# Optimization experiments

Hardware: AMD Instinct MI355X
Metric: run time of the kernel (lower is better)

Reference implementation:

```python
import jax, jax.numpy as jnp
import numpy as np

B, S, E, H = 4, 2048, 2048, 16
D = E // H  # head_dim = 128


def setup_inputs() -> dict:
    key = jax.random.key(0)
    ks = jax.random.split(key, 10)
    sc = 1.0 / np.sqrt(E)
    x = jax.random.normal(ks[0], (B, S, E), dtype=jnp.float32)
    causal_mask = jnp.tril(jnp.ones((S, S), dtype=jnp.int32))  # 1 = keep, 0 = mask
    wq = jax.random.normal(ks[1], (E, E), dtype=jnp.float32) * sc
    bq = jax.random.normal(ks[2], (E,), dtype=jnp.float32) * sc
    wk = jax.random.normal(ks[3], (E, E), dtype=jnp.float32) * sc
    bk = jax.random.normal(ks[4], (E,), dtype=jnp.float32) * sc
    wv = jax.random.normal(ks[5], (E, E), dtype=jnp.float32) * sc
    bv = jax.random.normal(ks[6], (E,), dtype=jnp.float32) * sc
    wo = jax.random.normal(ks[7], (E, E), dtype=jnp.float32) * sc
    bo = jax.random.normal(ks[8], (E,), dtype=jnp.float32) * sc
    return {"x": x, "causal_mask": causal_mask, "wq": wq, "bq": bq,
            "wk": wk, "bk": bk, "wv": wv, "bv": bv, "wo": wo, "bo": bo}


def _split_heads(t):
    # [B,S,E] -> [B,H,S,D]
    return t.reshape(B, S, H, D).transpose(0, 2, 1, 3)


def reference(x, causal_mask, wq, bq, wk, bk, wv, bv, wo, bo):
    # torch Linear: y = x @ W.T + b
    q = _split_heads(x @ wq.T + bq)
    k = _split_heads(x @ wk.T + bk)
    v = _split_heads(x @ wv.T + bv)
    scale = 1.0 / jnp.sqrt(jnp.asarray(D, dtype=x.dtype))
    dots = jnp.einsum("bhqd,bhkd->bhqk", q, k) * scale
    dots = jnp.where(causal_mask == 0, jnp.asarray(-jnp.inf, dots.dtype), dots)
    attn = jax.nn.softmax(dots, axis=-1)
    ctx = jnp.einsum("bhqk,bhkd->bhqd", attn, v)
    ctx = ctx.transpose(0, 2, 1, 3).reshape(B, S, E)  # merge heads
    return ctx @ wo.T + bo
```

## Files before the change

### kernel.cpp

```cpp
#include <hip/hip_runtime.h>
#include <hip/hip_bf16.h>

#define B_ 4
#define S_ 2048
#define E_ 2048
#define H_ 16
#define D_ 128
#define M_ (B_*S_)

typedef __attribute__((ext_vector_type(8))) short short8;
typedef __attribute__((ext_vector_type(4))) float f32x4;

__device__ __forceinline__ unsigned short f2bf(float f) {
  union { __hip_bfloat16 h; unsigned short u; } c;
  c.h = __float2bfloat16(f);
  return c.u;
}

__device__ __forceinline__ void gld_lds16(const void* g, void* l) {
  __builtin_amdgcn_global_load_lds((const __attribute__((address_space(1))) void*)g,
                                   (__attribute__((address_space(3))) void*)l, 16, 0, 0);
}

__global__ __launch_bounds__(256) void cast_bf16_kernel(const float* __restrict__ in,
                                                        unsigned short* __restrict__ out,
                                                        int n4) {
  int i = blockIdx.x * 256 + threadIdx.x;
  if (i >= n4) return;
  float4 v = ((const float4*)in)[i];
  ushort4 o;
  o.x = f2bf(v.x); o.y = f2bf(v.y); o.z = f2bf(v.z); o.w = f2bf(v.w);
  ((ushort4*)out)[i] = o;
}

template <typename OutT, bool TR = false>
__global__ __launch_bounds__(256) void gemm_bt(const unsigned short* __restrict__ A,
                                               const unsigned short* __restrict__ W,
                                               const float* __restrict__ bias,
                                               OutT* __restrict__ C,
                                               int M, int N, int K, float oscale) {
  __shared__ unsigned short As[128 * 64];
  __shared__ unsigned short Bs[128 * 64];
  const int tid  = threadIdx.x;
  const int lane = tid & 63;
  const int wid  = tid >> 6;
  const int nwg = gridDim.x * gridDim.y;
  const int lin = blockIdx.x + gridDim.x * blockIdx.y;
  const int nl  = (lin & 7) * (nwg >> 3) + (lin >> 3);
  const int m0 = (nl / gridDim.x) * 128;
  const int n0 = (nl % gridDim.x) * 128;
  const int wr = (wid >> 1) * 64;
  const int wc = (wid & 1) * 64;
  const int lr  = lane & 15;
  const int lg  = lane >> 4;

  f32x4 acc[4][4];
#pragma unroll
  for (int i = 0; i < 4; i++)
#pragma unroll
    for (int j = 0; j < 4; j++) acc[i][j] = (f32x4){0.f, 0.f, 0.f, 0.f};

  const int rS = tid >> 3;
  const int uS = (tid & 7) ^ (rS & 7);
  const unsigned short* asrc = A + (size_t)(m0 + rS) * K + uS * 8;
  const unsigned short* bsrc = W + (size_t)(n0 + rS) * K + uS * 8;
  char* adst = (char*)As + wid * 1024;
  char* bdst = (char*)Bs + wid * 1024;

  const int swR = (lr & 7) << 4;

  for (int kt = 0; kt < K; kt += 64) {
#pragma unroll
    for (int p = 0; p < 4; ++p) {
      gld_lds16(asrc + kt + (size_t)(32 * p) * K, adst + p * 4096);
      gld_lds16(bsrc + kt + (size_t)(32 * p) * K, bdst + p * 4096);
    }
    __syncthreads();

#pragma unroll
    for (int kk = 0; kk < 2; kk++) {
      const int cb = ((kk * 4 + lg) << 4) ^ swR;
      short8 af[4], bf[4];
#pragma unroll
      for (int i = 0; i < 4; i++)
        af[i] = *(const short8*)((const char*)As + (wr + i * 16 + lr) * 128 + cb);
#pragma unroll
      for (int j = 0; j < 4; j++)
        bf[j] = *(const short8*)((const char*)Bs + (wc + j * 16 + lr) * 128 + cb);
#pragma unroll
      for (int i = 0; i < 4; i++)
#pragma unroll
        for (int j = 0; j < 4; j++) {
          if constexpr (TR)
            acc[i][j] = __builtin_amdgcn_mfma_f32_16x16x32_bf16(bf[j], af[i], acc[i][j], 0, 0, 0);
          else
            acc[i][j] = __builtin_amdgcn_mfma_f32_16x16x32_bf16(af[i], bf[j], acc[i][j], 0, 0, 0);
        }
    }
    __syncthreads();
  }

  if constexpr (TR) {
    const int lg4 = (lane >> 4) * 4;
#pragma unroll
    for (int j = 0; j < 4; j++) {
      const int gn = n0 + wc + j * 16 + lg4;
      const float4 bv4 = *(const float4*)&bias[gn];
#pragma unroll
      for (int i = 0; i < 4; i++) {
        const int gm = m0 + wr + i * 16 + lr;
#pragma unroll
        for (int r = 0; r < 4; r++) {
          const float v = (acc[i][j][r] + ((const float*)&bv4)[r]) * oscale;
          ((unsigned short*)C)[(size_t)(gn + r) * M + gm] = f2bf(v);
        }
      }
    }
  } else {
#pragma unroll
    for (int i = 0; i < 4; i++) {
      const int gm = m0 + wr + i * 16 + (lane >> 4) * 4;
#pragma unroll
      for (int j = 0; j < 4; j++) {
        const int gn = n0 + wc + j * 16 + lr;
        const float bv = bias[gn];
#pragma unroll
        for (int r = 0; r < 4; r++) {
          const float v = (acc[i][j][r] + bv) * oscale;
          if constexpr (sizeof(OutT) == 2)
            ((unsigned short*)C)[(size_t)(gm + r) * N + gn] = f2bf(v);
          else
            ((float*)C)[(size_t)(gm + r) * N + gn] = v;
        }
      }
    }
  }
}

__global__ __launch_bounds__(256, 4) void flash_attn(const unsigned short* __restrict__ Q,
                                                     const unsigned short* __restrict__ K,
                                                     const unsigned short* __restrict__ VT,
                                                     unsigned short* __restrict__ Ctx) {
  __shared__ unsigned short Ks[64 * 128];
  __shared__ unsigned short Vt[128 * 64];
  __shared__ unsigned short Pl[4 * 1024];

  const int tid  = threadIdx.x;
  const int lane = tid & 63;
  const int wid  = tid >> 6;
  const int lr  = lane & 15;
  const int lg  = lane >> 4;
  const int lk8 = lg * 8;
  const int lin = blockIdx.x + 16 * blockIdx.y + 256 * blockIdx.z;
  const int nl  = (lin & 7) * 128 + (lin >> 3);
  const int bxw = nl & 15;
  const int h   = (nl >> 4) & 15;
  const int b   = nl >> 8;
  const size_t base = ((size_t)b * S_) * E_ + (size_t)h * D_;
  const unsigned short* __restrict__ Kh = K + base;
  const unsigned short* __restrict__ VTh = VT + (size_t)(h * D_) * M_ + (size_t)b * S_;
  unsigned short* Plf = Pl + wid * 1024;

  const int rK = tid >> 4;
  const int cK = ((tid * 16) & 255) ^ ((rK & 7) << 4);
  const unsigned short* ksrcB = Kh + (size_t)rK * E_ + (cK >> 1);
  char* kdstB = (char*)Ks + wid * 1024;

  const int dVb = tid >> 3;
  const int cV  = tid & 7;
  const unsigned short* vsrcB = VTh + (size_t)dVb * M_ + (size_t)((cV ^ (dVb & 7)) * 8);
  char* vdstB = (char*)Vt + wid * 1024;

  const int plw0 = (lg >> 1) * 128 + lr * 8 + (lg & 1) * 4;
  const int plrd = lg * 128 + lr * 8;

#pragma unroll 1
  for (int half = 0; half < 2; ++half) {
    const int ti = half ? (31 - bxw) : bxw;
    const int qblk = ti * 64;
    const int q0w  = qblk + wid * 16;
    const int qrow = q0w + lr;

    short8 qf[4];
#pragma unroll
    for (int kk = 0; kk < 4; kk++)
      qf[kk] = *(const short8*)&Q[base + (size_t)qrow * E_ + kk * 32 + lk8];

    f32x4 o[8];
#pragma unroll
    for (int d0 = 0; d0 < 8; d0++) o[d0] = (f32x4){0.f, 0.f, 0.f, 0.f};
    float mrow = -INFINITY;
    float lsum = 0.f;

    const int nt = ti + 1;

    for (int t = 0; t < nt; ++t) {
      const int kv0 = t * 64;
      const size_t koff = (size_t)kv0 * E_;

#pragma unroll
      for (int p = 0; p < 4; ++p) {
        gld_lds16(ksrcB + koff + (size_t)(16 * p) * E_, kdstB + p * 4096);
        gld_lds16(vsrcB + (size_t)(32 * p) * M_ + kv0,  vdstB + p * 4096);
      }
      __syncthreads();

      f32x4 s[4];
#pragma unroll
      for (int c = 0; c < 4; c++) s[c] = (f32x4){0.f, 0.f, 0.f, 0.f};
      const int swK = (lr & 7) << 4;
      __builtin_amdgcn_s_setprio(1);
#pragma unroll
      for (int kk = 0; kk < 4; kk++) {
        const int cb = (kk * 64 + lg * 16) ^ swK;
#pragma unroll
        for (int c = 0; c < 4; c++) {
          const short8 kf = *(const short8*)((const char*)Ks + (c * 16 + lr) * 256 + cb);
          s[c] = __builtin_amdgcn_mfma_f32_16x16x32_bf16(kf, qf[kk], s[c], 0, 0, 0);
        }
      }
      __builtin_amdgcn_s_setprio(0);

      float v[4][4];
#pragma unroll
      for (int c = 0; c < 4; c++)
#pragma unroll
        for (int r = 0; r < 4; r++) v[c][r] = s[c][r];
      if (t == nt - 1) {
#pragma unroll
        for (int c = 0; c < 4; c++) {
          const int kvq = kv0 + c * 16 + lg * 4;
#pragma unroll
          for (int r = 0; r < 4; r++)
            if (kvq + r > qrow) v[c][r] = -INFINITY;
        }
      }

      float pm = fmaxf(fmaxf(fmaxf(v[0][0], v[0][1]), fmaxf(v[0][2], v[0][3])),
                       fmaxf(fmaxf(v[1][0], v[1][1]), fmaxf(v[1][2], v[1][3])));
      pm = fmaxf(pm, fmaxf(fmaxf(fmaxf(v[2][0], v[2][1]), fmaxf(v[2][2], v[2][3])),
                           fmaxf(fmaxf(v[3][0], v[3][1]), fmaxf(v[3][2], v[3][3]))));
      pm = fmaxf(pm, __shfl_xor(pm, 16));
      pm = fmaxf(pm, __shfl_xor(pm, 32));

      const float need = pm - mrow;
      if (!__all(need <= 8.f)) {
        const float mnew = fmaxf(mrow, pm);
        const float al = __expf(mrow - mnew);
        lsum *= al;
#pragma unroll
        for (int d0 = 0; d0 < 8; ++d0) {
          f32x4 tt = o[d0];
          tt[0] *= al; tt[1] *= al; tt[2] *= al; tt[3] *= al;
          o[d0] = tt;
        }
        mrow = mnew;
      }

      ushort4 wpk[4];
      float ps = 0.f;
#pragma unroll
      for (int c = 0; c < 4; c++) {
        const float e0 = __expf(v[c][0] - mrow);
        const float e1 = __expf(v[c][1] - mrow);
        const float e2 = __expf(v[c][2] - mrow);
        const float e3 = __expf(v[c][3] - mrow);
        wpk[c].x = f2bf(e0); wpk[c].y = f2bf(e1);
        wpk[c].z = f2bf(e2); wpk[c].w = f2bf(e3);
        ps += (e0 + e1) + (e2 + e3);
      }
      lsum += ps;

#pragma unroll
      for (int c = 0; c < 4; c++)
        *(ushort4*)&Plf[plw0 + c * 256] = wpk[c];
      asm volatile("s_waitcnt lgkmcnt(0)" ::: "memory");
      __builtin_amdgcn_sched_barrier(0);

      const short8 pb0 = *(const short8*)&Plf[plrd];
      const short8 pb1 = *(const short8*)&Plf[plrd + 512];
      const int d7 = lr & 7;
      __builtin_amdgcn_s_setprio(1);
#pragma unroll
      for (int d0 = 0; d0 < 8; ++d0) {
        const int d = d0 * 16 + lr;
        const short8 vb0 = *(const short8*)&Vt[d * 64 + ((lg ^ d7) << 3)];
        o[d0] = __builtin_amdgcn_mfma_f32_16x16x32_bf16(vb0, pb0, o[d0], 0, 0, 0);
        const short8 vb1 = *(const short8*)&Vt[d * 64 + (((4 + lg) ^ d7) << 3)];
        o[d0] = __builtin_amdgcn_mfma_f32_16x16x32_bf16(vb1, pb1, o[d0], 0, 0, 0);
      }
      __builtin_amdgcn_s_setprio(0);
      __syncthreads();
    }

    float ls = lsum;
    ls += __shfl_xor(ls, 16);
    ls += __shfl_xor(ls, 32);
    const float inv = 1.0f / ls;
    unsigned short* crow = Ctx + base + (size_t)qrow * E_ + lg * 4;
#pragma unroll
    for (int d0 = 0; d0 < 8; ++d0) {
      ushort4 st;
      st.x = f2bf(o[d0][0] * inv);
      st.y = f2bf(o[d0][1] * inv);
      st.z = f2bf(o[d0][2] * inv);
      st.w = f2bf(o[d0][3] * inv);
      *(ushort4*)&crow[d0 * 16] = st;
    }
  }
}

extern "C" void kernel_launch(void* const* d_in, const int* in_sizes, int n_in,
                              void* d_out, int out_size, void* d_ws, size_t ws_size,
                              hipStream_t stream) {
  const float* x  = (const float*)d_in[0];
  const float* wq = (const float*)d_in[2];
  const float* bq = (const float*)d_in[3];
  const float* wk = (const float*)d_in[4];
  const float* bk = (const float*)d_in[5];
  const float* wv = (const float*)d_in[6];
  const float* bv = (const float*)d_in[7];
  const float* wo = (const float*)d_in[8];
  const float* bo = (const float*)d_in[9];
  float* out = (float*)d_out;

  char* ws = (char*)d_ws;
  const size_t MB = 1024 * 1024;
  unsigned short* xb  = (unsigned short*)(ws);
  unsigned short* wqb = (unsigned short*)(ws + 32 * MB);
  unsigned short* wkb = (unsigned short*)(ws + 40 * MB);
  unsigned short* wvb = (unsigned short*)(ws + 48 * MB);
  unsigned short* wob = (unsigned short*)(ws + 56 * MB);
  unsigned short* Qb  = (unsigned short*)(ws + 64 * MB);
  unsigned short* Kb  = (unsigned short*)(ws + 96 * MB);
  unsigned short* VTb = (unsigned short*)(ws + 128 * MB);
  unsigned short* Cb  = (unsigned short*)(ws + 160 * MB);

  const int nx4 = M_ * E_ / 4;
  const int nw4 = E_ * E_ / 4;
  cast_bf16_kernel<<<nx4 / 256, 256, 0, stream>>>(x,  xb,  nx4);
  cast_bf16_kernel<<<nw4 / 256, 256, 0, stream>>>(wq, wqb, nw4);
  cast_bf16_kernel<<<nw4 / 256, 256, 0, stream>>>(wk, wkb, nw4);
  cast_bf16_kernel<<<nw4 / 256, 256, 0, stream>>>(wv, wvb, nw4);
  cast_bf16_kernel<<<nw4 / 256, 256, 0, stream>>>(wo, wob, nw4);

  const float scale = 0.08838834764831845f;
  dim3 gg(E_ / 128, M_ / 128);
  gemm_bt<unsigned short><<<gg, 256, 0, stream>>>(xb, wqb, bq, Qb, M_, E_, E_, scale);
  gemm_bt<unsigned short><<<gg, 256, 0, stream>>>(xb, wkb, bk, Kb, M_, E_, E_, 1.0f);
  gemm_bt<unsigned short, true><<<gg, 256, 0, stream>>>(xb, wvb, bv, VTb, M_, E_, E_, 1.0f);

  flash_attn<<<dim3(S_ / 64 / 2, H_, B_), 256, 0, stream>>>(Qb, Kb, VTb, Cb);

  gemm_bt<float><<<gg, 256, 0, stream>>>(Cb, wob, bo, out, M_, E_, E_, 1.0f);
}
```

Baseline: 494.3 us.

## Enlarge GEMM tiles to 256x256 with double-buffered LDS prefetch

```diff
diff --git a/kernel.cpp b/kernel.cpp
--- a/kernel.cpp
+++ b/kernel.cpp
@@ -34,29 +34,29 @@
 }
 
 template <typename OutT, bool TR = false>
-__global__ __launch_bounds__(256) void gemm_bt(const unsigned short* __restrict__ A,
-                                               const unsigned short* __restrict__ W,
-                                               const float* __restrict__ bias,
-                                               OutT* __restrict__ C,
-                                               int M, int N, int K, float oscale) {
-  __shared__ unsigned short As[128 * 64];
-  __shared__ unsigned short Bs[128 * 64];
+__global__ __launch_bounds__(512) void gemm_bt256(const unsigned short* __restrict__ A,
+                                                  const unsigned short* __restrict__ W,
+                                                  const float* __restrict__ bias,
+                                                  OutT* __restrict__ C,
+                                                  int M, int N, int K, float oscale) {
+  __shared__ unsigned short As[2 * 256 * 64];
+  __shared__ unsigned short Bs[2 * 256 * 64];
   const int tid  = threadIdx.x;
   const int lane = tid & 63;
   const int wid  = tid >> 6;
   const int nwg = gridDim.x * gridDim.y;
   const int lin = blockIdx.x + gridDim.x * blockIdx.y;
   const int nl  = (lin & 7) * (nwg >> 3) + (lin >> 3);
-  const int m0 = (nl / gridDim.x) * 128;
-  const int n0 = (nl % gridDim.x) * 128;
-  const int wr = (wid >> 1) * 64;
-  const int wc = (wid & 1) * 64;
+  const int m0 = (nl / gridDim.x) * 256;
+  const int n0 = (nl % gridDim.x) * 256;
+  const int wr = (wid >> 2) * 128;
+  const int wc = (wid & 3) * 64;
   const int lr  = lane & 15;
   const int lg  = lane >> 4;
 
-  f32x4 acc[4][4];
-#pragma unroll
-  for (int i = 0; i < 4; i++)
+  f32x4 acc[8][4];
+#pragma unroll
+  for (int i = 0; i < 8; i++)
 #pragma unroll
     for (int j = 0; j < 4; j++) acc[i][j] = (f32x4){0.f, 0.f, 0.f, 0.f};
 
@@ -68,46 +68,66 @@
   char* bdst = (char*)Bs + wid * 1024;
 
   const int swR = (lr & 7) << 4;
-
-  for (int kt = 0; kt < K; kt += 64) {
-#pragma unroll
-    for (int p = 0; p < 4; ++p) {
-      gld_lds16(asrc + kt + (size_t)(32 * p) * K, adst + p * 4096);
-      gld_lds16(bsrc + kt + (size_t)(32 * p) * K, bdst + p * 4096);
-    }
+  const int nK = K >> 6;
+
+#pragma unroll
+  for (int i = 0; i < 4; ++i) {
+    gld_lds16(asrc + (size_t)(64 * i) * K, adst + i * 8192);
+    gld_lds16(bsrc + (size_t)(64 * i) * K, bdst + i * 8192);
+  }
+
+  for (int t = 0; t < nK; ++t) {
+    const int bo = (t & 1) * 32768;
     __syncthreads();
 
+    if (t + 1 < nK) {
+      const int kt2 = (t + 1) * 64;
+      const int nbo = bo ^ 32768;
+#pragma unroll
+      for (int i = 0; i < 4; ++i) {
+        gld_lds16(asrc + kt2 + (size_t)(64 * i) * K, adst + nbo + i * 8192);
+        gld_lds16(bsrc + kt2 + (size_t)(64 * i) * K, bdst + nbo + i * 8192);
+      }
+    }
+
+    const char* AsB = (const char*)As + bo;
+    const char* BsB = (const char*)Bs + bo;
 #pragma unroll
     for (int kk = 0; kk < 2; kk++) {
       const int cb = ((kk * 4 + lg) << 4) ^ swR;
-      short8 af[4], bf[4];
-#pragma unroll
-      for (int i = 0; i < 4; i++)
-        af[i] = *(const short8*)((const char*)As + (wr + i * 16 + lr) * 128 + cb);
+      short8 bf[4];
 #pragma unroll
       for (int j = 0; j < 4; j++)
-        bf[j] = *(const short8*)((const char*)Bs + (wc + j * 16 + lr) * 128 + cb);
-#pragma unroll
-      for (int i = 0; i < 4; i++)
-#pragma unroll
-        for (int j = 0; j < 4; j++) {
-          if constexpr (TR)
-            acc[i][j] = __builtin_amdgcn_mfma_f32_16x16x32_bf16(bf[j], af[i], acc[i][j], 0, 0, 0);
-          else
-            acc[i][j] = __builtin_amdgcn_mfma_f32_16x16x32_bf16(af[i], bf[j], acc[i][j], 0, 0, 0);
-        }
-    }
-    __syncthreads();
+        bf[j] = *(const short8*)(BsB + (wc + j * 16 + lr) * 128 + cb);
+#pragma unroll
+      for (int mh = 0; mh < 2; mh++) {
+        short8 af[4];
+#pragma unroll
+        for (int i = 0; i < 4; i++)
+          af[i] = *(const short8*)(AsB + (wr + mh * 64 + i * 16 + lr) * 128 + cb);
+        __builtin_amdgcn_s_setprio(1);
+#pragma unroll
+        for (int i = 0; i < 4; i++)
+#pragma unroll
+          for (int j = 0; j < 4; j++) {
+            if constexpr (TR)
+              acc[mh * 4 + i][j] = __builtin_amdgcn_mfma_f32_16x16x32_bf16(bf[j], af[i], acc[mh * 4 + i][j], 0, 0, 0);
+            else
+              acc[mh * 4 + i][j] = __builtin_amdgcn_mfma_f32_16x16x32_bf16(af[i], bf[j], acc[mh * 4 + i][j], 0, 0, 0);
+          }
+        __builtin_amdgcn_s_setprio(0);
+      }
+    }
   }
 
   if constexpr (TR) {
-    const int lg4 = (lane >> 4) * 4;
+    const int lg4 = lg * 4;
 #pragma unroll
     for (int j = 0; j < 4; j++) {
       const int gn = n0 + wc + j * 16 + lg4;
       const float4 bv4 = *(const float4*)&bias[gn];
 #pragma unroll
-      for (int i = 0; i < 4; i++) {
+      for (int i = 0; i < 8; i++) {
         const int gm = m0 + wr + i * 16 + lr;
 #pragma unroll
         for (int r = 0; r < 4; r++) {
@@ -118,8 +138,8 @@
     }
   } else {
 #pragma unroll
-    for (int i = 0; i < 4; i++) {
-      const int gm = m0 + wr + i * 16 + (lane >> 4) * 4;
+    for (int i = 0; i < 8; i++) {
+      const int gm = m0 + wr + i * 16 + lg * 4;
 #pragma unroll
       for (int j = 0; j < 4; j++) {
         const int gn = n0 + wc + j * 16 + lr;
@@ -345,12 +365,12 @@
   cast_bf16_kernel<<<nw4 / 256, 256, 0, stream>>>(wo, wob, nw4);
 
   const float scale = 0.08838834764831845f;
-  dim3 gg(E_ / 128, M_ / 128);
-  gemm_bt<unsigned short><<<gg, 256, 0, stream>>>(xb, wqb, bq, Qb, M_, E_, E_, scale);
-  gemm_bt<unsigned short><<<gg, 256, 0, stream>>>(xb, wkb, bk, Kb, M_, E_, E_, 1.0f);
-  gemm_bt<unsigned short, true><<<gg, 256, 0, stream>>>(xb, wvb, bv, VTb, M_, E_, E_, 1.0f);
+  dim3 gg(E_ / 256, M_ / 256);
+  gemm_bt256<unsigned short><<<gg, 512, 0, stream>>>(xb, wqb, bq, Qb, M_, E_, E_, scale);
+  gemm_bt256<unsigned short><<<gg, 512, 0, stream>>>(xb, wkb, bk, Kb, M_, E_, E_, 1.0f);
+  gemm_bt256<unsigned short, true><<<gg, 512, 0, stream>>>(xb, wvb, bv, VTb, M_, E_, E_, 1.0f);
 
   flash_attn<<<dim3(S_ / 64 / 2, H_, B_), 256, 0, stream>>>(Qb, Kb, VTb, Cb);
 
-  gemm_bt<float><<<gg, 256, 0, stream>>>(Cb, wob, bo, out, M_, E_, E_, 1.0f);
-}
+  gemm_bt256<float><<<gg, 512, 0, stream>>>(Cb, wob, bo, out, M_, E_, E_, 1.0f);
+}
```

After: 420.1 us. 15.0% less time.
